# Kernel tuning notes

Measured on AMD Instinct MI355X. Metric: run time of the kernel, lower is better.

## Reference

```python
import jax, jax.numpy as jnp
import numpy as np

NUM_NODES = 512
NUM_EDGES = 512
EMB_DIM = 128
HIDDEN = 256
NUM_INC = 8192


def setup_inputs() -> dict:
    key = jax.random.key(0)
    ks = jax.random.split(key, 8)
    X = jax.random.normal(ks[0], (NUM_NODES, EMB_DIM), dtype=jnp.float32)
    V = jax.random.randint(ks[1], (NUM_INC,), 0, NUM_NODES, dtype=jnp.int64)
    E = jax.random.randint(ks[2], (NUM_INC,), 0, NUM_EDGES, dtype=jnp.int64)
    # MLP params, torch nn.Linear layout: W (out, in), y = x @ W.T + b
    lim1 = 1.0 / np.sqrt(2 * EMB_DIM)
    W1 = jax.random.uniform(ks[3], (HIDDEN, 2 * EMB_DIM), minval=-lim1, maxval=lim1, dtype=jnp.float32)
    b1 = jax.random.uniform(ks[4], (HIDDEN,), minval=-lim1, maxval=lim1, dtype=jnp.float32)
    lim2 = 1.0 / np.sqrt(HIDDEN)
    W2 = jax.random.uniform(ks[5], (1, HIDDEN), minval=-lim2, maxval=lim2, dtype=jnp.float32)
    b2 = jax.random.uniform(ks[6], (1,), minval=-lim2, maxval=lim2, dtype=jnp.float32)
    return {"X": X, "V": V, "E": E, "W1": W1, "b1": b1, "W2": W2, "b2": b2}


def reference(X, V, E, W1, b1, W2, b2):
    d = X.shape[-1]
    # scatter-mean of gathered node embeddings into edges; empty edges -> 0 (nan_to_num)
    sums = jax.ops.segment_sum(X[V], E, num_segments=NUM_EDGES)          # (M, d)
    cnt = jax.ops.segment_sum(jnp.ones((V.shape[0],), X.dtype), E, num_segments=NUM_EDGES)
    eX = jnp.where(cnt[:, None] > 0, sums / jnp.maximum(cnt[:, None], 1.0), 0.0)
    # cat([X_expanded, eX_expanded]) @ W1.T == X @ W1[:, :d].T + eX @ W1[:, d:].T (broadcast add)
    hX = X @ W1[:, :d].T                                                 # (N, H)
    hE = eX @ W1[:, d:].T                                                # (M, H)
    hidden = jax.nn.relu(hX[:, None, :] + hE[None, :, :] + b1)           # (N, M, H)
    logits = jnp.einsum('nmh,h->nm', hidden, W2[0]) + b2[0]              # (N, M)
    prob = jax.nn.sigmoid(logits)
    prob = jnp.nan_to_num(prob, nan=0.5)
    prob = jnp.clip(prob, 1e-6, 1.0 - 1e-6)
    return prob
```

## Files before the change

### kernel.cpp

```cpp
#include <hip/hip_runtime.h>
#include <math.h>

#define NN 512
#define MM 512
#define DD 128
#define HH 256

typedef float v4f __attribute__((ext_vector_type(4)));

#define WS_A 0
#define WS_C (NN * HH)

__global__ __launch_bounds__(256) void k_stage(
    const float* __restrict__ X, const int* __restrict__ V,
    const int* __restrict__ E, const float* __restrict__ W1,
    const float* __restrict__ b1, float* __restrict__ A,
    float* __restrict__ C, int ninc)
{
    __shared__ int   lst[8192];
    __shared__ float eXp[2 * DD];
    __shared__ float eXs[DD];
    __shared__ int   cnt_s;

    const int b = blockIdx.x;
    const int t = threadIdx.x;

    if (b < MM) {
        if (t == 0) cnt_s = 0;
        __syncthreads();
        const int nq = ninc >> 2;
        for (int c = t; c < nq; c += 256) {
            int4 e4 = ((const int4*)E)[c];
            int base = c * 4;
            if (e4.x == b) lst[atomicAdd(&cnt_s, 1)] = base + 0;
            if (e4.y == b) lst[atomicAdd(&cnt_s, 1)] = base + 1;
            if (e4.z == b) lst[atomicAdd(&cnt_s, 1)] = base + 2;
            if (e4.w == b) lst[atomicAdd(&cnt_s, 1)] = base + 3;
        }
        __syncthreads();
        const int cnt = cnt_s;

        const int d = t & 127, half = t >> 7;
        float a0 = 0.f, a1 = 0.f;
        int j = half;
        for (; j + 2 < cnt; j += 4) {
            int i0 = lst[j], i1 = lst[j + 2];
            a0 += X[V[i0] * DD + d];
            a1 += X[V[i1] * DD + d];
        }
        for (; j < cnt; j += 2) a0 += X[V[lst[j]] * DD + d];
        eXp[half * DD + d] = a0 + a1;
        __syncthreads();
        if (t < DD) {
            float inv = cnt > 0 ? 1.0f / (float)cnt : 0.0f;
            eXs[t] = (eXp[t] + eXp[DD + t]) * inv;
        }
        __syncthreads();

        const float* w = W1 + t * (2 * DD) + DD;
        v4f dv = (v4f)(0.f);
        #pragma unroll 8
        for (int k = 0; k < DD; k += 4)
            dv += (*(const v4f*)(w + k)) * (*(const v4f*)(eXs + k));
        C[b * HH + t] = b1[t] + dv.x + dv.y + dv.z + dv.w;
    } else {
        const int r0 = (b - MM) * 4;
        const float* w  = W1 + t * (2 * DD);
        const float* x0 = X + (r0 + 0) * DD;
        const float* x1 = X + (r0 + 1) * DD;
        const float* x2 = X + (r0 + 2) * DD;
        const float* x3 = X + (r0 + 3) * DD;
        v4f acc0 = (v4f)(0.f), acc1 = (v4f)(0.f), acc2 = (v4f)(0.f), acc3 = (v4f)(0.f);
        #pragma unroll 4
        for (int k = 0; k < DD; k += 4) {
            v4f wv = *(const v4f*)(w + k);
            acc0 += wv * (*(const v4f*)(x0 + k));
            acc1 += wv * (*(const v4f*)(x1 + k));
            acc2 += wv * (*(const v4f*)(x2 + k));
            acc3 += wv * (*(const v4f*)(x3 + k));
        }
        A[(r0 + 0) * HH + t] = acc0.x + acc0.y + acc0.z + acc0.w;
        A[(r0 + 1) * HH + t] = acc1.x + acc1.y + acc1.z + acc1.w;
        A[(r0 + 2) * HH + t] = acc2.x + acc2.y + acc2.z + acc2.w;
        A[(r0 + 3) * HH + t] = acc3.x + acc3.y + acc3.z + acc3.w;
    }
}

__global__ __launch_bounds__(256) void k_pairs(
    const float* __restrict__ A, const float* __restrict__ C,
    const float* __restrict__ W2, const float* __restrict__ b2,
    float* __restrict__ out)
{
    __shared__ float lds[8192];
    const int tid = threadIdx.x;
    const int bx  = blockIdx.x;
    const int tn0 = (bx >> 5) * 16;
    const int tm0 = (bx & 31) * 16;

    {
        const int c0 = (tid & 63) * 4;
        const int rw = tid >> 6;
        #pragma unroll
        for (int p = 0; p < 4; ++p) {
            int r  = p * 4 + rw;
            int sh = c0 ^ (r & 28);
            *(float4*)&lds[r * 256 + sh]        = *(const float4*)&A[(tn0 + r) * HH + c0];
            *(float4*)&lds[4096 + r * 256 + sh] = *(const float4*)&C[(tm0 + r) * HH + c0];
        }
    }
    __syncthreads();

    const int w = tid >> 6, lane = tid & 63;
    const int ra = 2 * (lane & 7);
    const int rc = 2 * (lane >> 3);
    const int pa = ra & 28, pc = rc & 28;
    const int h0 = w * 64;

    v4f s00 = (v4f)(0.f), s01 = (v4f)(0.f), s10 = (v4f)(0.f), s11 = (v4f)(0.f);
    const v4f z = (v4f)(0.f);
    const float* la = lds + ra * 256;
    const float* lc = lds + 4096 + rc * 256;

    #pragma unroll 4
    for (int hh = 0; hh < 64; hh += 4) {
        int h = h0 + hh;
        v4f wv  = *(const v4f*)(W2 + h);
        v4f av0 = *(const v4f*)(la + (h ^ pa));
        v4f av1 = *(const v4f*)(la + 256 + (h ^ pa));
        v4f cv0 = *(const v4f*)(lc + (h ^ pc));
        v4f cv1 = *(const v4f*)(lc + 256 + (h ^ pc));
        s00 += wv * __builtin_elementwise_max(av0 + cv0, z);
        s01 += wv * __builtin_elementwise_max(av0 + cv1, z);
        s10 += wv * __builtin_elementwise_max(av1 + cv0, z);
        s11 += wv * __builtin_elementwise_max(av1 + cv1, z);
    }
    float a00 = s00.x + s00.y + s00.z + s00.w;
    float a01 = s01.x + s01.y + s01.z + s01.w;
    float a10 = s10.x + s10.y + s10.z + s10.w;
    float a11 = s11.x + s11.y + s11.z + s11.w;

    __syncthreads();
    lds[w * 256 + (ra + 0) * 16 + (rc + 0)] = a00;
    lds[w * 256 + (ra + 0) * 16 + (rc + 1)] = a01;
    lds[w * 256 + (ra + 1) * 16 + (rc + 0)] = a10;
    lds[w * 256 + (ra + 1) * 16 + (rc + 1)] = a11;
    __syncthreads();

    const int p = tid;
    float s = lds[p] + lds[256 + p] + lds[512 + p] + lds[768 + p] + b2[0];
    float prob = 1.0f / (1.0f + __expf(-s));
    prob = fminf(fmaxf(prob, 1e-6f), 1.0f - 1e-6f);
    out[(tn0 + (p >> 4)) * MM + tm0 + (p & 15)] = prob;
}

extern "C" void kernel_launch(void* const* d_in, const int* in_sizes, int n_in,
                              void* d_out, int out_size, void* d_ws, size_t ws_size,
                              hipStream_t stream)
{
    const float* X  = (const float*)d_in[0];
    const int*   V  = (const int*)d_in[1];
    const int*   E  = (const int*)d_in[2];
    const float* W1 = (const float*)d_in[3];
    const float* b1 = (const float*)d_in[4];
    const float* W2 = (const float*)d_in[5];
    const float* b2 = (const float*)d_in[6];

    float* ws  = (float*)d_ws;
    float* A   = ws + WS_A;
    float* C   = ws + WS_C;
    float* out = (float*)d_out;
    int ninc   = in_sizes[1];

    k_stage<<<MM + NN / 4, 256, 0, stream>>>(X, V, E, W1, b1, A, C, ninc);
    k_pairs<<<(NN / 16) * (MM / 16), 256, 0, stream>>>(A, C, W2, b2, out);
}
```

Measured before the change: 88.49 us.

## Store hidden projections in fp16 and use packed fdot2 in pair kernel

The intermediate node and edge projections A and C are now stored as fp16. The pair kernel loads them into padded LDS rows, does the add and ReLU in packed half precision, and reduces against W2 with the fdot2 intrinsic into fp32 accumulators. This halves intermediate memory traffic and LDS footprint and doubles arithmetic throughput per instruction. The stage kernel also resolves V indices while building the incidence list, which removes one dependent global load per gathered row. The cost is lower precision in the hidden activations, which could perturb the output probabilities.

```diff
diff --git a/kernel.cpp b/kernel.cpp
--- a/kernel.cpp
+++ b/kernel.cpp
@@ -6,16 +6,16 @@
 #define DD 128
 #define HH 256
 
-typedef float v4f __attribute__((ext_vector_type(4)));
+typedef float     v4f __attribute__((ext_vector_type(4)));
+typedef _Float16  h8  __attribute__((ext_vector_type(8)));
+typedef _Float16  h2  __attribute__((ext_vector_type(2)));
 
-#define WS_A 0
-#define WS_C (NN * HH)
 
 __global__ __launch_bounds__(256) void k_stage(
     const float* __restrict__ X, const int* __restrict__ V,
     const int* __restrict__ E, const float* __restrict__ W1,
-    const float* __restrict__ b1, float* __restrict__ A,
-    float* __restrict__ C, int ninc)
+    const float* __restrict__ b1, _Float16* __restrict__ A,
+    _Float16* __restrict__ C, int ninc)
 {
     __shared__ int   lst[8192];
     __shared__ float eXp[2 * DD];
@@ -32,10 +32,10 @@
         for (int c = t; c < nq; c += 256) {
             int4 e4 = ((const int4*)E)[c];
             int base = c * 4;
-            if (e4.x == b) lst[atomicAdd(&cnt_s, 1)] = base + 0;
-            if (e4.y == b) lst[atomicAdd(&cnt_s, 1)] = base + 1;
-            if (e4.z == b) lst[atomicAdd(&cnt_s, 1)] = base + 2;
-            if (e4.w == b) lst[atomicAdd(&cnt_s, 1)] = base + 3;
+            if (e4.x == b) lst[atomicAdd(&cnt_s, 1)] = V[base + 0];
+            if (e4.y == b) lst[atomicAdd(&cnt_s, 1)] = V[base + 1];
+            if (e4.z == b) lst[atomicAdd(&cnt_s, 1)] = V[base + 2];
+            if (e4.w == b) lst[atomicAdd(&cnt_s, 1)] = V[base + 3];
         }
         __syncthreads();
         const int cnt = cnt_s;
@@ -44,11 +44,11 @@
         float a0 = 0.f, a1 = 0.f;
         int j = half;
         for (; j + 2 < cnt; j += 4) {
-            int i0 = lst[j], i1 = lst[j + 2];
-            a0 += X[V[i0] * DD + d];
-            a1 += X[V[i1] * DD + d];
+            int v0 = lst[j], v1 = lst[j + 2];
+            a0 += X[v0 * DD + d];
+            a1 += X[v1 * DD + d];
         }
-        for (; j < cnt; j += 2) a0 += X[V[lst[j]] * DD + d];
+        for (; j < cnt; j += 2) a0 += X[lst[j] * DD + d];
         eXp[half * DD + d] = a0 + a1;
         __syncthreads();
         if (t < DD) {
@@ -62,7 +62,7 @@
         #pragma unroll 8
         for (int k = 0; k < DD; k += 4)
             dv += (*(const v4f*)(w + k)) * (*(const v4f*)(eXs + k));
-        C[b * HH + t] = b1[t] + dv.x + dv.y + dv.z + dv.w;
+        C[b * HH + t] = (_Float16)(b1[t] + dv.x + dv.y + dv.z + dv.w);
     } else {
         const int r0 = (b - MM) * 4;
         const float* w  = W1 + t * (2 * DD);
@@ -79,75 +79,84 @@
             acc2 += wv * (*(const v4f*)(x2 + k));
             acc3 += wv * (*(const v4f*)(x3 + k));
         }
-        A[(r0 + 0) * HH + t] = acc0.x + acc0.y + acc0.z + acc0.w;
-        A[(r0 + 1) * HH + t] = acc1.x + acc1.y + acc1.z + acc1.w;
-        A[(r0 + 2) * HH + t] = acc2.x + acc2.y + acc2.z + acc2.w;
-        A[(r0 + 3) * HH + t] = acc3.x + acc3.y + acc3.z + acc3.w;
+        A[(r0 + 0) * HH + t] = (_Float16)(acc0.x + acc0.y + acc0.z + acc0.w);
+        A[(r0 + 1) * HH + t] = (_Float16)(acc1.x + acc1.y + acc1.z + acc1.w);
+        A[(r0 + 2) * HH + t] = (_Float16)(acc2.x + acc2.y + acc2.z + acc2.w);
+        A[(r0 + 3) * HH + t] = (_Float16)(acc3.x + acc3.y + acc3.z + acc3.w);
     }
 }
 
+#define ROWH 264
+#define CT   (16 * ROWH)
+#define WT   (32 * ROWH)
+
+__device__ inline float dot8(h8 w, h8 a, h8 c, float acc) {
+    h8 s = a + c;
+    s = __builtin_elementwise_max(s, (h8)(_Float16)0.f);
+    union { h8 v; h2 p[4]; } su, wu;
+    su.v = s; wu.v = w;
+    acc = __builtin_amdgcn_fdot2(su.p[0], wu.p[0], acc, false);
+    acc = __builtin_amdgcn_fdot2(su.p[1], wu.p[1], acc, false);
+    acc = __builtin_amdgcn_fdot2(su.p[2], wu.p[2], acc, false);
+    acc = __builtin_amdgcn_fdot2(su.p[3], wu.p[3], acc, false);
+    return acc;
+}
+
 __global__ __launch_bounds__(256) void k_pairs(
-    const float* __restrict__ A, const float* __restrict__ C,
+    const _Float16* __restrict__ A, const _Float16* __restrict__ C,
     const float* __restrict__ W2, const float* __restrict__ b2,
     float* __restrict__ out)
 {
-    __shared__ float lds[8192];
-    const int tid = threadIdx.x;
-    const int bx  = blockIdx.x;
+    __shared__ _Float16 lds[WT + 256];
+    const int t  = threadIdx.x;
+    const int bx = blockIdx.x;
     const int tn0 = (bx >> 5) * 16;
     const int tm0 = (bx & 31) * 16;
 
-    {
-        const int c0 = (tid & 63) * 4;
-        const int rw = tid >> 6;
-        #pragma unroll
-        for (int p = 0; p < 4; ++p) {
-            int r  = p * 4 + rw;
-            int sh = c0 ^ (r & 28);
-            *(float4*)&lds[r * 256 + sh]        = *(const float4*)&A[(tn0 + r) * HH + c0];
-            *(float4*)&lds[4096 + r * 256 + sh] = *(const float4*)&C[(tm0 + r) * HH + c0];
-        }
+    lds[WT + t] = (_Float16)W2[t];
+    #pragma unroll
+    for (int p = 0; p < 4; ++p) {
+        int g = p * 256 + t;
+        int row = g >> 5, c8 = (g & 31) * 8;
+        const _Float16* src;
+        int dst;
+        if (row < 16) { src = A + (tn0 + row) * HH + c8;        dst = row * ROWH + c8; }
+        else          { src = C + (tm0 + row - 16) * HH + c8;   dst = CT + (row - 16) * ROWH + c8; }
+        *(h8*)&lds[dst] = *(const h8*)src;
     }
     __syncthreads();
 
-    const int w = tid >> 6, lane = tid & 63;
+    const int w = t >> 6, lane = t & 63;
     const int ra = 2 * (lane & 7);
     const int rc = 2 * (lane >> 3);
-    const int pa = ra & 28, pc = rc & 28;
-    const int h0 = w * 64;
+    const _Float16* la = lds + ra * ROWH + w * 64;
+    const _Float16* lc = lds + CT + rc * ROWH + w * 64;
+    const _Float16* lw = lds + WT + w * 64;
 
-    v4f s00 = (v4f)(0.f), s01 = (v4f)(0.f), s10 = (v4f)(0.f), s11 = (v4f)(0.f);
-    const v4f z = (v4f)(0.f);
-    const float* la = lds + ra * 256;
-    const float* lc = lds + 4096 + rc * 256;
-
-    #pragma unroll 4
-    for (int hh = 0; hh < 64; hh += 4) {
-        int h = h0 + hh;
-        v4f wv  = *(const v4f*)(W2 + h);
-        v4f av0 = *(const v4f*)(la + (h ^ pa));
-        v4f av1 = *(const v4f*)(la + 256 + (h ^ pa));
-        v4f cv0 = *(const v4f*)(lc + (h ^ pc));
-        v4f cv1 = *(const v4f*)(lc + 256 + (h ^ pc));
-        s00 += wv * __builtin_elementwise_max(av0 + cv0, z);
-        s01 += wv * __builtin_elementwise_max(av0 + cv1, z);
-        s10 += wv * __builtin_elementwise_max(av1 + cv0, z);
-        s11 += wv * __builtin_elementwise_max(av1 + cv1, z);
+    float a00 = 0.f, a01 = 0.f, a10 = 0.f, a11 = 0.f;
+    #pragma unroll
+    for (int hh = 0; hh < 64; hh += 8) {
+        h8 wv  = *(const h8*)(lw + hh);
+        h8 av0 = *(const h8*)(la + hh);
+        h8 av1 = *(const h8*)(la + ROWH + hh);
+        h8 cv0 = *(const h8*)(lc + hh);
+        h8 cv1 = *(const h8*)(lc + ROWH + hh);
+        a00 = dot8(wv, av0, cv0, a00);
+        a01 = dot8(wv, av0, cv1, a01);
+        a10 = dot8(wv, av1, cv0, a10);
+        a11 = dot8(wv, av1, cv1, a11);
     }
-    float a00 = s00.x + s00.y + s00.z + s00.w;
-    float a01 = s01.x + s01.y + s01.z + s01.w;
-    float a10 = s10.x + s10.y + s10.z + s10.w;
-    float a11 = s11.x + s11.y + s11.z + s11.w;
 
     __syncthreads();
-    lds[w * 256 + (ra + 0) * 16 + (rc + 0)] = a00;
-    lds[w * 256 + (ra + 0) * 16 + (rc + 1)] = a01;
-    lds[w * 256 + (ra + 1) * 16 + (rc + 0)] = a10;
-    lds[w * 256 + (ra + 1) * 16 + (rc + 1)] = a11;
+    float* red = (float*)lds;
+    red[w * 256 + (ra + 0) * 16 + (rc + 0)] = a00;
+    red[w * 256 + (ra + 0) * 16 + (rc + 1)] = a01;
+    red[w * 256 + (ra + 1) * 16 + (rc + 0)] = a10;
+    red[w * 256 + (ra + 1) * 16 + (rc + 1)] = a11;
     __syncthreads();
 
-    const int p = tid;
-    float s = lds[p] + lds[256 + p] + lds[512 + p] + lds[768 + p] + b2[0];
+    const int p = t;
+    float s = red[p] + red[256 + p] + red[512 + p] + red[768 + p] + b2[0];
     float prob = 1.0f / (1.0f + __expf(-s));
     prob = fminf(fmaxf(prob, 1e-6f), 1.0f - 1e-6f);
     out[(tn0 + (p >> 4)) * MM + tm0 + (p & 15)] = prob;
@@ -165,11 +174,10 @@
     const float* W2 = (const float*)d_in[5];
     const float* b2 = (const float*)d_in[6];
 
-    float* ws  = (float*)d_ws;
-    float* A   = ws + WS_A;
-    float* C   = ws + WS_C;
-    float* out = (float*)d_out;
-    int ninc   = in_sizes[1];
+    _Float16* A = (_Float16*)d_ws;
+    _Float16* C = A + NN * HH;
+    float* out  = (float*)d_out;
+    int ninc    = in_sizes[1];
 
     k_stage<<<MM + NN / 4, 256, 0, stream>>>(X, V, E, W1, b1, A, C, ninc);
     k_pairs<<<(NN / 16) * (MM / 16), 256, 0, stream>>>(A, C, W2, b2, out);
```

Measured after the change: 85.11 us. 1.04x faster.
